# Kernel optimization log

Measured on AMD Instinct MI355X. Metric: run time of the kernel, lower is better.

## Reference

```python
import jax, jax.numpy as jnp
import numpy as np

N_EMBD = 1024
N_HEAD = 16

def setup_inputs() -> dict:
    key = jax.random.key(0)
    ks = jax.random.split(key, 6)
    C = N_EMBD
    s = 1.0 / np.sqrt(C)
    x = jax.random.normal(ks[0], (4, 2048, C), dtype=jnp.float32)
    Wk = jax.random.normal(ks[1], (C, C), dtype=jnp.float32) * s
    Wq = jax.random.normal(ks[2], (C, C), dtype=jnp.float32) * s
    Wv = jax.random.normal(ks[3], (C, C), dtype=jnp.float32) * s
    Wp = jax.random.normal(ks[4], (C, C), dtype=jnp.float32) * s
    bp = jax.random.normal(ks[5], (C,), dtype=jnp.float32) * 0.01
    return {"x": x, "Wq": Wq, "Wk": Wk, "Wv": Wv, "Wp": Wp, "bp": bp}

def reference(x, Wq, Wk, Wv, Wp, bp):
    B, T, C = x.shape
    H = N_HEAD
    d = C // H
    # projections (bias=False)
    q = (x @ Wq).reshape(B, T, H, d).transpose(0, 2, 1, 3)  # [B,H,T,d]
    k = (x @ Wk).reshape(B, T, H, d).transpose(0, 2, 1, 3)
    v = (x @ Wv).reshape(B, T, H, d).transpose(0, 2, 1, 3)
    att = jnp.einsum('bhqd,bhkd->bhqk', q, k) * (1.0 / np.sqrt(d))
    causal = jnp.tril(jnp.ones((T, T), dtype=bool))
    att = jnp.where(causal[None, None], att, jnp.float32(-jnp.inf))
    att = jax.nn.softmax(att, axis=-1)
    y = jnp.einsum('bhqk,bhkd->bhqd', att, v)  # [B,H,T,d]
    y = y.transpose(0, 2, 1, 3).reshape(B, T, C)
    return y @ Wp + bp
```

## Files before the change

kernel.cpp:

```cpp
#include <hip/hip_runtime.h>
#include <hip/hip_bf16.h>

#define N_EMBD 1024
#define N_HEADS 16
#define HD 64
#define TSEQ 2048
#define BATCH 4
#define M_TOT (BATCH*TSEQ)

typedef short s16x8 __attribute__((ext_vector_type(8)));
typedef float f32x4 __attribute__((ext_vector_type(4)));

__device__ __forceinline__ void glds16(const void* g, void* l) {
  __builtin_amdgcn_global_load_lds((const __attribute__((address_space(1))) void*)g,
                                   (__attribute__((address_space(3))) void*)l, 16, 0, 0);
}

__device__ __forceinline__ float exp_scaled(float s) {
  float r;
  asm("v_exp_f32 %0, %1\n\ts_nop 0" : "=v"(r) : "v"(s * 0.18033688011112042f));
  return r;
}

__global__ __launch_bounds__(256) void xcast_kernel(const float* __restrict__ x,
                                                    __hip_bfloat16* __restrict__ xb) {
  int i = blockIdx.x * 256 + threadIdx.x;
  float4 f = ((const float4*)x)[i];
  __hip_bfloat162 p0, p1;
  p0.x = __float2bfloat16(f.x); p0.y = __float2bfloat16(f.y);
  p1.x = __float2bfloat16(f.z); p1.y = __float2bfloat16(f.w);
  ((__hip_bfloat162*)xb)[2*i]   = p0;
  ((__hip_bfloat162*)xb)[2*i+1] = p1;
}

__global__ void wcast_kernel(const float* __restrict__ Wq, const float* __restrict__ Wk,
                             const float* __restrict__ Wv, const float* __restrict__ Wp,
                             __hip_bfloat16* __restrict__ wqkvt, __hip_bfloat16* __restrict__ wpt) {
  __shared__ float tile[32][33];
  int z = blockIdx.z;
  const float* in = (z==0)?Wq:(z==1)?Wk:(z==2)?Wv:Wp;
  __hip_bfloat16* out = (z<3) ? (wqkvt + (size_t)z*N_EMBD*N_EMBD) : wpt;
  int tx = threadIdx.x, ty = threadIdx.y;
  int x  = blockIdx.x*32 + tx;
  int y0 = blockIdx.y*32;
  #pragma unroll
  for (int j=0;j<4;++j) tile[ty + j*8][tx] = in[(size_t)(y0+ty+j*8)*N_EMBD + x];
  __syncthreads();
  int xo  = y0 + tx;
  int yo0 = blockIdx.x*32;
  #pragma unroll
  for (int j=0;j<4;++j)
    out[(size_t)(yo0+ty+j*8)*N_EMBD + xo] = __float2bfloat16(tile[tx][ty+j*8]);
}

__global__ __launch_bounds__(256) void gemm_kernel(
    const __hip_bfloat16* __restrict__ A,
    const __hip_bfloat16* __restrict__ Bt,
    __hip_bfloat16* __restrict__ Qb, __hip_bfloat16* __restrict__ Kb,
    __hip_bfloat16* __restrict__ Vt,
    float* __restrict__ out, const float* __restrict__ bias, int mode) {
  __shared__ __align__(16) char smem[32768];
  __hip_bfloat16* Alin = (__hip_bfloat16*)smem;
  __hip_bfloat16* Blin = (__hip_bfloat16*)(smem + 16384);
  int tid = threadIdx.x;
  int m0 = blockIdx.y*128, n0 = blockIdx.x*128;
  int w = tid>>6, lane = tid&63, l16 = lane&15, quad = lane>>4;
  int wr = w>>1, wc = w&1;
  int xg = l16 & 7;
  int off0 = ((quad    ) ^ xg)*8;
  int off1 = ((quad + 4) ^ xg)*8;
  f32x4 acc[4][4];
  #pragma unroll
  for (int mi=0;mi<4;++mi)
    #pragma unroll
    for (int ni=0;ni<4;++ni) acc[mi][ni] = (f32x4){0.f,0.f,0.f,0.f};

  for (int k0=0; k0<N_EMBD; k0+=64) {
    __syncthreads();
    #pragma unroll
    for (int rd=0; rd<4; ++rd) {
      int slot = rd*256 + tid;
      int row  = slot>>3;
      int gc8  = ((tid&7) ^ (row&7))*8;
      glds16(A  + (size_t)(m0+row)*N_EMBD + k0 + gc8, Alin + slot*8);
      glds16(Bt + (size_t)(n0+row)*N_EMBD + k0 + gc8, Blin + slot*8);
    }
    __syncthreads();
    #pragma unroll
    for (int c=0;c<2;++c) {
      int off = c ? off1 : off0;
      s16x8 af[4], bfr[4];
      #pragma unroll
      for (int mi=0;mi<4;++mi)
        af[mi] = *(const s16x8*)(Alin + (wr*64+mi*16+l16)*64 + off);
      #pragma unroll
      for (int ni=0;ni<4;++ni)
        bfr[ni] = *(const s16x8*)(Blin + (wc*64+ni*16+l16)*64 + off);
      #pragma unroll
      for (int mi=0;mi<4;++mi)
        #pragma unroll
        for (int ni=0;ni<4;++ni)
          acc[mi][ni] = __builtin_amdgcn_mfma_f32_16x16x32_bf16(af[mi], bfr[ni], acc[mi][ni],0,0,0);
    }
  }

  if (mode == 0) {
    int which = n0 >> 10;
    int bb = m0 >> 11, t0 = m0 & 2047;
    if (which < 2) {
      __hip_bfloat16* outp = (which==0)?Qb:Kb;
      #pragma unroll
      for (int mi=0;mi<4;++mi) {
        #pragma unroll
        for (int ni=0;ni<4;++ni) {
          int ncol = (n0 & 1023) + wc*64 + ni*16 + l16;
          int hh = ncol>>6, dd = ncol&63;
          #pragma unroll
          for (int r=0;r<4;++r) {
            int t = t0 + wr*64 + mi*16 + quad*4 + r;
            outp[((size_t)(bb*N_HEADS + hh)*TSEQ + t)*HD + dd] = __float2bfloat16(acc[mi][ni][r]);
          }
        }
      }
    } else {
      int hh0 = (n0 & 1023) >> 6;
      __hip_bfloat16 (*Ts)[136] = (__hip_bfloat16(*)[136])smem;
      #pragma unroll
      for (int p=0;p<2;++p) {
        __syncthreads();
        if (wc == p) {
          #pragma unroll
          for (int mi=0;mi<4;++mi)
            #pragma unroll
            for (int ni=0;ni<4;++ni) {
              int dd = ni*16 + l16;
              #pragma unroll
              for (int r=0;r<4;++r)
                Ts[dd][wr*64 + mi*16 + quad*4 + r] = __float2bfloat16(acc[mi][ni][r]);
            }
        }
        __syncthreads();
        int dd = tid>>2, tc = (tid&3)*32;
        __hip_bfloat16* dst = Vt + ((size_t)(bb*N_HEADS + hh0 + p)*HD + dd)*TSEQ + t0 + tc;
        #pragma unroll
        for (int c4=0;c4<4;++c4)
          *(uint4*)(dst + c4*8) = *(const uint4*)&Ts[dd][tc + c4*8];
      }
    }
  } else {
    #pragma unroll
    for (int mi=0;mi<4;++mi) {
      #pragma unroll
      for (int ni=0;ni<4;++ni) {
        int col = n0 + wc*64 + ni*16 + l16;
        float bs = bias[col];
        #pragma unroll
        for (int r=0;r<4;++r) {
          int m = m0 + wr*64 + mi*16 + quad*4 + r;
          out[(size_t)m*N_EMBD + col] = acc[mi][ni][r] + bs;
        }
      }
    }
  }
}

#define PST 68
__global__ __launch_bounds__(256) void attn_kernel(
    const __hip_bfloat16* __restrict__ Qb, const __hip_bfloat16* __restrict__ Kb,
    const __hip_bfloat16* __restrict__ Vt, __hip_bfloat16* __restrict__ Yb) {
  __shared__ __align__(16) __hip_bfloat16 Ks[2][64][64];
  __shared__ __align__(16) __hip_bfloat16 Vs[2][64][64];
  __shared__ __align__(16) __hip_bfloat16 Ps[128][PST];
  int tid = threadIdx.x;
  int b = blockIdx.z, h = blockIdx.y;
  int qb = (b & 1) ? (TSEQ/128 - 1 - blockIdx.x) : blockIdx.x;
  int q0 = qb*128;
  size_t bhT  = (size_t)(b*N_HEADS + h)*TSEQ;
  size_t bhHD = (size_t)(b*N_HEADS + h)*HD;
  int lane = tid&63, w = tid>>6, l16 = lane&15, quad = lane>>4;
  int wq = w*32;
  int xg = l16 & 7;
  int off0 = ((quad    ) ^ xg)*8;
  int off1 = ((quad + 4) ^ xg)*8;

  int slot0 = tid,        row0 = slot0>>3, gcA = ((tid&7) ^ (row0&7))*8;
  int slot1 = 256 + tid,  row1 = slot1>>3, gcB = ((tid&7) ^ (row1&7))*8;

  s16x8 qf[2][2];
  #pragma unroll
  for (int mi=0;mi<2;++mi) {
    const __hip_bfloat16* qrow = Qb + (bhT + q0 + wq + mi*16 + l16)*HD;
    qf[mi][0] = *(const s16x8*)(qrow + quad*8);
    qf[mi][1] = *(const s16x8*)(qrow + 32 + quad*8);
  }

  f32x4 z4 = {0.f,0.f,0.f,0.f};
  f32x4 oacc[4][2];
  #pragma unroll
  for (int ni=0;ni<4;++ni) { oacc[ni][0]=z4; oacc[ni][1]=z4; }
  float lrow[2][4] = {{0.f,0.f,0.f,0.f},{0.f,0.f,0.f,0.f}};

  int ntiles = 2*qb + 2;

  {
    glds16(Kb + (bhT + 0 + row0)*HD + gcA,    &Ks[0][0][0] + slot0*8);
    glds16(Vt + (bhHD + row0)*TSEQ + 0 + gcA, &Vs[0][0][0] + slot0*8);
    glds16(Kb + (bhT + 0 + row1)*HD + gcB,    &Ks[0][0][0] + slot1*8);
    glds16(Vt + (bhHD + row1)*TSEQ + 0 + gcB, &Vs[0][0][0] + slot1*8);
  }

  for (int t=0; t<ntiles; ++t) {
    int cur = t&1;
    int k0 = t*64;
    if (t+1 < ntiles) {
      int kn = k0 + 64;
      glds16(Kb + (bhT + kn + row0)*HD + gcA,     &Ks[cur^1][0][0] + slot0*8);
      glds16(Vt + (bhHD + row0)*TSEQ + kn + gcA,  &Vs[cur^1][0][0] + slot0*8);
      glds16(Kb + (bhT + kn + row1)*HD + gcB,     &Ks[cur^1][0][0] + slot1*8);
      glds16(Vt + (bhHD + row1)*TSEQ + kn + gcB,  &Vs[cur^1][0][0] + slot1*8);
      asm volatile("s_waitcnt vmcnt(4)" ::: "memory");
    } else {
      asm volatile("s_waitcnt vmcnt(0)" ::: "memory");
    }
    __builtin_amdgcn_s_barrier();
    __builtin_amdgcn_sched_barrier(0);

    const __hip_bfloat16* Kc = &Ks[cur][0][0];
    const __hip_bfloat16* Vc = &Vs[cur][0][0];

    f32x4 sacc[4][2];
    #pragma unroll
    for (int ni=0; ni<4; ++ni) {
      s16x8 kb0 = *(const s16x8*)(Kc + (ni*16+l16)*64 + off0);
      s16x8 kb1 = *(const s16x8*)(Kc + (ni*16+l16)*64 + off1);
      #pragma unroll
      for (int mi=0; mi<2; ++mi) {
        f32x4 s = z4;
        s = __builtin_amdgcn_mfma_f32_16x16x32_bf16(qf[mi][0], kb0, s,0,0,0);
        s = __builtin_amdgcn_mfma_f32_16x16x32_bf16(qf[mi][1], kb1, s,0,0,0);
        sacc[ni][mi] = s;
      }
    }

    if (q0 + wq >= k0 + 63) {
      #pragma unroll
      for (int ni=0; ni<4; ++ni) {
        #pragma unroll
        for (int mi=0; mi<2; ++mi) {
          #pragma unroll
          for (int r=0; r<4; ++r) {
            float p = exp_scaled(sacc[ni][mi][r]);
            lrow[mi][r] += p;
            Ps[wq + mi*16 + quad*4 + r][ni*16 + l16] = __float2bfloat16(p);
          }
        }
      }
    } else {
      #pragma unroll
      for (int ni=0; ni<4; ++ni) {
        int kcol = k0 + ni*16 + l16;
        #pragma unroll
        for (int mi=0; mi<2; ++mi) {
          int qrb = q0 + wq + mi*16 + quad*4;
          #pragma unroll
          for (int r=0; r<4; ++r) {
            float e = exp_scaled(sacc[ni][mi][r]);
            float p = (qrb + r >= kcol) ? e : 0.f;
            lrow[mi][r] += p;
            Ps[wq + mi*16 + quad*4 + r][ni*16 + l16] = __float2bfloat16(p);
          }
        }
      }
    }

    union U8 { s16x8 v; uint2 u[2]; };
    U8 aP[2][2];
    #pragma unroll
    for (int mi=0; mi<2; ++mi)
      #pragma unroll
      for (int c=0; c<2; ++c) {
        const __hip_bfloat16* pr = &Ps[wq + mi*16 + l16][c*32 + quad*8];
        aP[mi][c].u[0] = *(const uint2*)pr;
        aP[mi][c].u[1] = *(const uint2*)(pr + 4);
      }
    #pragma unroll
    for (int ni=0; ni<4; ++ni) {
      s16x8 vb0 = *(const s16x8*)(Vc + (ni*16+l16)*64 + off0);
      s16x8 vb1 = *(const s16x8*)(Vc + (ni*16+l16)*64 + off1);
      #pragma unroll
      for (int mi=0; mi<2; ++mi) {
        oacc[ni][mi] = __builtin_amdgcn_mfma_f32_16x16x32_bf16(aP[mi][0].v, vb0, oacc[ni][mi],0,0,0);
        oacc[ni][mi] = __builtin_amdgcn_mfma_f32_16x16x32_bf16(aP[mi][1].v, vb1, oacc[ni][mi],0,0,0);
      }
    }

    asm volatile("s_waitcnt lgkmcnt(0)" ::: "memory");
    __builtin_amdgcn_s_barrier();
    __builtin_amdgcn_sched_barrier(0);
  }

  #pragma unroll
  for (int off=1; off<16; off<<=1)
    #pragma unroll
    for (int mi=0; mi<2; ++mi)
      #pragma unroll
      for (int r=0; r<4; ++r) lrow[mi][r] += __shfl_xor(lrow[mi][r], off);

  #pragma unroll
  for (int mi=0; mi<2; ++mi)
    #pragma unroll
    for (int r=0; r<4; ++r) {
      float inv = 1.f / lrow[mi][r];
      int tq = q0 + wq + mi*16 + quad*4 + r;
      __hip_bfloat16* yr = Yb + ((size_t)(b*TSEQ + tq))*N_EMBD + h*HD;
      #pragma unroll
      for (int ni=0; ni<4; ++ni)
        yr[ni*16 + l16] = __float2bfloat16(oacc[ni][mi][r] * inv);
    }
}

extern "C" void kernel_launch(void* const* d_in, const int* in_sizes, int n_in,
                              void* d_out, int out_size, void* d_ws, size_t ws_size,
                              hipStream_t stream) {
  const float* x  = (const float*)d_in[0];
  const float* Wq = (const float*)d_in[1];
  const float* Wk = (const float*)d_in[2];
  const float* Wv = (const float*)d_in[3];
  const float* Wp = (const float*)d_in[4];
  const float* bp = (const float*)d_in[5];

  char* w = (char*)d_ws;
  __hip_bfloat16* xb    = (__hip_bfloat16*)w;  w += (size_t)M_TOT*N_EMBD*2;
  __hip_bfloat16* wqkvt = (__hip_bfloat16*)w;  w += (size_t)3*N_EMBD*N_EMBD*2;
  __hip_bfloat16* wpt   = (__hip_bfloat16*)w;  w += (size_t)N_EMBD*N_EMBD*2;
  __hip_bfloat16* Qb    = (__hip_bfloat16*)w;  w += (size_t)M_TOT*N_EMBD*2;
  __hip_bfloat16* Kb    = (__hip_bfloat16*)w;  w += (size_t)M_TOT*N_EMBD*2;
  __hip_bfloat16* Vt    = (__hip_bfloat16*)w;  w += (size_t)M_TOT*N_EMBD*2;
  __hip_bfloat16* Yb    = (__hip_bfloat16*)w;

  xcast_kernel<<<dim3(M_TOT*N_EMBD/1024), dim3(256), 0, stream>>>(x, xb);
  wcast_kernel<<<dim3(32,32,4), dim3(32,8), 0, stream>>>(Wq,Wk,Wv,Wp,wqkvt,wpt);
  gemm_kernel<<<dim3(24,64), dim3(256), 0, stream>>>(xb, wqkvt, Qb,Kb,Vt, nullptr, nullptr, 0);
  attn_kernel<<<dim3(TSEQ/128,N_HEADS,BATCH), dim3(256), 0, stream>>>(Qb,Kb,Vt,Yb);
  gemm_kernel<<<dim3(8,64), dim3(256), 0, stream>>>(Yb, wpt, nullptr,nullptr,nullptr,
                                                    (float*)d_out, bp, 1);
}
```

Before: 278.1 us.

## Keep softmax probabilities in registers by computing transposed scores in attention

```diff
diff --git a/kernel.cpp b/kernel.cpp
--- a/kernel.cpp
+++ b/kernel.cpp
@@ -19,6 +19,12 @@
 __device__ __forceinline__ float exp_scaled(float s) {
   float r;
   asm("v_exp_f32 %0, %1\n\ts_nop 0" : "=v"(r) : "v"(s * 0.18033688011112042f));
+  return r;
+}
+
+__device__ __forceinline__ unsigned cvtpk(float lo, float hi) {
+  unsigned r;
+  asm("v_cvt_pk_bf16_f32 %0, %1, %2" : "=v"(r) : "v"(lo), "v"(hi));
   return r;
 }
 
@@ -164,13 +170,11 @@
   }
 }
 
-#define PST 68
 __global__ __launch_bounds__(256) void attn_kernel(
     const __hip_bfloat16* __restrict__ Qb, const __hip_bfloat16* __restrict__ Kb,
     const __hip_bfloat16* __restrict__ Vt, __hip_bfloat16* __restrict__ Yb) {
   __shared__ __align__(16) __hip_bfloat16 Ks[2][64][64];
   __shared__ __align__(16) __hip_bfloat16 Vs[2][64][64];
-  __shared__ __align__(16) __hip_bfloat16 Ps[128][PST];
   int tid = threadIdx.x;
   int b = blockIdx.z, h = blockIdx.y;
   int qb = (b & 1) ? (TSEQ/128 - 1 - blockIdx.x) : blockIdx.x;
@@ -182,6 +186,12 @@
   int xg = l16 & 7;
   int off0 = ((quad    ) ^ xg)*8;
   int off1 = ((quad + 4) ^ xg)*8;
+  int q21 = quad>>1, q1 = (quad&1)*4;
+  int vo[2][2];
+  vo[0][0] = ((0 + q21) ^ xg)*8 + q1;
+  vo[0][1] = ((2 + q21) ^ xg)*8 + q1;
+  vo[1][0] = ((4 + q21) ^ xg)*8 + q1;
+  vo[1][1] = ((6 + q21) ^ xg)*8 + q1;
 
   int slot0 = tid,        row0 = slot0>>3, gcA = ((tid&7) ^ (row0&7))*8;
   int slot1 = 256 + tid,  row1 = slot1>>3, gcB = ((tid&7) ^ (row1&7))*8;
@@ -197,8 +207,8 @@
   f32x4 z4 = {0.f,0.f,0.f,0.f};
   f32x4 oacc[4][2];
   #pragma unroll
-  for (int ni=0;ni<4;++ni) { oacc[ni][0]=z4; oacc[ni][1]=z4; }
-  float lrow[2][4] = {{0.f,0.f,0.f,0.f},{0.f,0.f,0.f,0.f}};
+  for (int nd=0;nd<4;++nd) { oacc[nd][0]=z4; oacc[nd][1]=z4; }
+  float lsum[2] = {0.f, 0.f};
 
   int ntiles = 2*qb + 2;
 
@@ -236,61 +246,61 @@
       #pragma unroll
       for (int mi=0; mi<2; ++mi) {
         f32x4 s = z4;
-        s = __builtin_amdgcn_mfma_f32_16x16x32_bf16(qf[mi][0], kb0, s,0,0,0);
-        s = __builtin_amdgcn_mfma_f32_16x16x32_bf16(qf[mi][1], kb1, s,0,0,0);
+        s = __builtin_amdgcn_mfma_f32_16x16x32_bf16(kb0, qf[mi][0], s,0,0,0);
+        s = __builtin_amdgcn_mfma_f32_16x16x32_bf16(kb1, qf[mi][1], s,0,0,0);
         sacc[ni][mi] = s;
       }
     }
 
+    unsigned pkw[2][4][2];
     if (q0 + wq >= k0 + 63) {
       #pragma unroll
       for (int ni=0; ni<4; ++ni) {
         #pragma unroll
         for (int mi=0; mi<2; ++mi) {
-          #pragma unroll
-          for (int r=0; r<4; ++r) {
-            float p = exp_scaled(sacc[ni][mi][r]);
-            lrow[mi][r] += p;
-            Ps[wq + mi*16 + quad*4 + r][ni*16 + l16] = __float2bfloat16(p);
-          }
+          float e0 = exp_scaled(sacc[ni][mi][0]);
+          float e1 = exp_scaled(sacc[ni][mi][1]);
+          float e2 = exp_scaled(sacc[ni][mi][2]);
+          float e3 = exp_scaled(sacc[ni][mi][3]);
+          lsum[mi] += (e0+e1)+(e2+e3);
+          pkw[mi][ni][0] = cvtpk(e0, e1);
+          pkw[mi][ni][1] = cvtpk(e2, e3);
         }
       }
     } else {
       #pragma unroll
       for (int ni=0; ni<4; ++ni) {
-        int kcol = k0 + ni*16 + l16;
+        int kbase = k0 + ni*16 + quad*4;
         #pragma unroll
         for (int mi=0; mi<2; ++mi) {
-          int qrb = q0 + wq + mi*16 + quad*4;
-          #pragma unroll
-          for (int r=0; r<4; ++r) {
-            float e = exp_scaled(sacc[ni][mi][r]);
-            float p = (qrb + r >= kcol) ? e : 0.f;
-            lrow[mi][r] += p;
-            Ps[wq + mi*16 + quad*4 + r][ni*16 + l16] = __float2bfloat16(p);
-          }
-        }
-      }
-    }
-
-    union U8 { s16x8 v; uint2 u[2]; };
-    U8 aP[2][2];
-    #pragma unroll
-    for (int mi=0; mi<2; ++mi)
-      #pragma unroll
-      for (int c=0; c<2; ++c) {
-        const __hip_bfloat16* pr = &Ps[wq + mi*16 + l16][c*32 + quad*8];
-        aP[mi][c].u[0] = *(const uint2*)pr;
-        aP[mi][c].u[1] = *(const uint2*)(pr + 4);
-      }
-    #pragma unroll
-    for (int ni=0; ni<4; ++ni) {
-      s16x8 vb0 = *(const s16x8*)(Vc + (ni*16+l16)*64 + off0);
-      s16x8 vb1 = *(const s16x8*)(Vc + (ni*16+l16)*64 + off1);
-      #pragma unroll
-      for (int mi=0; mi<2; ++mi) {
-        oacc[ni][mi] = __builtin_amdgcn_mfma_f32_16x16x32_bf16(aP[mi][0].v, vb0, oacc[ni][mi],0,0,0);
-        oacc[ni][mi] = __builtin_amdgcn_mfma_f32_16x16x32_bf16(aP[mi][1].v, vb1, oacc[ni][mi],0,0,0);
+          int qrow = q0 + wq + mi*16 + l16;
+          float e0 = (qrow >= kbase    ) ? exp_scaled(sacc[ni][mi][0]) : 0.f;
+          float e1 = (qrow >= kbase + 1) ? exp_scaled(sacc[ni][mi][1]) : 0.f;
+          float e2 = (qrow >= kbase + 2) ? exp_scaled(sacc[ni][mi][2]) : 0.f;
+          float e3 = (qrow >= kbase + 3) ? exp_scaled(sacc[ni][mi][3]) : 0.f;
+          lsum[mi] += (e0+e1)+(e2+e3);
+          pkw[mi][ni][0] = cvtpk(e0, e1);
+          pkw[mi][ni][1] = cvtpk(e2, e3);
+        }
+      }
+    }
+
+    union U8 { s16x8 v; unsigned u[4]; uint2 u2[2]; };
+    #pragma unroll
+    for (int c=0; c<2; ++c) {
+      U8 pf0, pf1;
+      pf0.u[0] = pkw[0][2*c][0];   pf0.u[1] = pkw[0][2*c][1];
+      pf0.u[2] = pkw[0][2*c+1][0]; pf0.u[3] = pkw[0][2*c+1][1];
+      pf1.u[0] = pkw[1][2*c][0];   pf1.u[1] = pkw[1][2*c][1];
+      pf1.u[2] = pkw[1][2*c+1][0]; pf1.u[3] = pkw[1][2*c+1][1];
+      #pragma unroll
+      for (int nd=0; nd<4; ++nd) {
+        const __hip_bfloat16* vrow = Vc + (nd*16 + l16)*64;
+        U8 vf;
+        vf.u2[0] = *(const uint2*)(vrow + vo[c][0]);
+        vf.u2[1] = *(const uint2*)(vrow + vo[c][1]);
+        oacc[nd][0] = __builtin_amdgcn_mfma_f32_16x16x32_bf16(vf.v, pf0.v, oacc[nd][0],0,0,0);
+        oacc[nd][1] = __builtin_amdgcn_mfma_f32_16x16x32_bf16(vf.v, pf1.v, oacc[nd][1],0,0,0);
       }
     }
 
@@ -300,23 +310,24 @@
   }
 
   #pragma unroll
-  for (int off=1; off<16; off<<=1)
-    #pragma unroll
-    for (int mi=0; mi<2; ++mi)
-      #pragma unroll
-      for (int r=0; r<4; ++r) lrow[mi][r] += __shfl_xor(lrow[mi][r], off);
-
-  #pragma unroll
-  for (int mi=0; mi<2; ++mi)
-    #pragma unroll
-    for (int r=0; r<4; ++r) {
-      float inv = 1.f / lrow[mi][r];
-      int tq = q0 + wq + mi*16 + quad*4 + r;
-      __hip_bfloat16* yr = Yb + ((size_t)(b*TSEQ + tq))*N_EMBD + h*HD;
-      #pragma unroll
-      for (int ni=0; ni<4; ++ni)
-        yr[ni*16 + l16] = __float2bfloat16(oacc[ni][mi][r] * inv);
-    }
+  for (int mi=0; mi<2; ++mi) {
+    lsum[mi] += __shfl_xor(lsum[mi], 16);
+    lsum[mi] += __shfl_xor(lsum[mi], 32);
+  }
+
+  #pragma unroll
+  for (int mi=0; mi<2; ++mi) {
+    float inv = 1.f / lsum[mi];
+    int tq = q0 + wq + mi*16 + l16;
+    __hip_bfloat16* yr = Yb + ((size_t)(b*TSEQ + tq))*N_EMBD + h*HD + quad*4;
+    #pragma unroll
+    for (int nd=0; nd<4; ++nd) {
+      uint2 o;
+      o.x = cvtpk(oacc[nd][mi][0]*inv, oacc[nd][mi][1]*inv);
+      o.y = cvtpk(oacc[nd][mi][2]*inv, oacc[nd][mi][3]*inv);
+      *(uint2*)(yr + nd*16) = o;
+    }
+  }
 }
 
 extern "C" void kernel_launch(void* const* d_in, const int* in_sizes, int n_in,
```

Result: faster. 270.8 us (-2.6%).
